# Optimization experiments

Hardware: AMD Instinct MI355X
Metric: run time of the kernel (lower is better)

The kernel has to match this reference:

```python
import jax, jax.numpy as jnp
import numpy as np

D_EMB = 1024
N_HEADS = 16
HEAD_DIM = D_EMB // N_HEADS


def _xavier(key, out_f, in_f):
    limit = jnp.sqrt(6.0 / (in_f + out_f))
    return jax.random.uniform(key, (out_f, in_f), jnp.float32, -limit, limit)


def setup_inputs() -> dict:
    key = jax.random.key(0)
    k_x, k_qkv, k_out = jax.random.split(key, 3)
    x = jax.random.normal(k_x, (4, 2048, D_EMB), jnp.float32)
    # torch nn.Linear weights: [out_features, in_features], xavier_uniform; biases zero
    w_qkv = _xavier(k_qkv, 3 * D_EMB, D_EMB)
    b_qkv = jnp.zeros((3 * D_EMB,), jnp.float32)
    w_out = _xavier(k_out, D_EMB, D_EMB)
    b_out = jnp.zeros((D_EMB,), jnp.float32)
    return {"x": x, "w_qkv": w_qkv, "b_qkv": b_qkv, "w_out": w_out, "b_out": b_out}


def reference(x, w_qkv, b_qkv, w_out, b_out):
    B, S, D = x.shape
    # QKV projection: y = x @ W^T + b -> [B, S, 3D]
    qkv = jnp.einsum('bsd,ed->bse', x, w_qkv) + b_qkv
    # view(B, S, H, 3*head_dim) then split into q, k, v (matches torch chunk on last dim)
    qkv = qkv.reshape(B, S, N_HEADS, 3 * HEAD_DIM)
    q, k, v = jnp.split(qkv, 3, axis=-1)  # each [B, S, H, head_dim]
    scale = 1.0 / jnp.sqrt(jnp.float32(HEAD_DIM))
    scores = jnp.einsum('bshd,bthd->bhst', q, k) * scale  # [B, H, S, S]
    probs = jax.nn.softmax(scores, axis=-1)
    out = jnp.einsum('bhst,bthd->bshd', probs, v).reshape(B, S, D)
    return jnp.einsum('bsd,ed->bse', out, w_out) + b_out
```

## Files before the change

### kernel.cpp

```cpp
#include <hip/hip_runtime.h>

typedef __bf16 bf16_t;
typedef __bf16 bf16x8 __attribute__((ext_vector_type(8)));
typedef __bf16 bf16x4 __attribute__((ext_vector_type(4)));
typedef float f32x4 __attribute__((ext_vector_type(4)));

#define S_LEN 2048
#define D_EMB 1024
#define NH 16

#define MFMA16(a, b, c) __builtin_amdgcn_mfma_f32_16x16x32_bf16((a), (b), (c), 0, 0, 0)

__device__ __forceinline__ void gld16(void* lds, const void* g) {
  __builtin_amdgcn_global_load_lds(
      (__attribute__((address_space(1))) void*)(void*)(g),
      (__attribute__((address_space(3))) void*)(lds), 16, 0, 0);
}

__device__ __forceinline__ float exp2_hw(float x) {
  float r;
  asm("v_exp_f32 %0, %1" : "=v"(r) : "v"(x));
  return r;
}

__global__ __launch_bounds__(256) void cvt_bf16(const float* __restrict__ in,
                                                bf16_t* __restrict__ out, int n4) {
  int i = blockIdx.x * 256 + threadIdx.x;
  if (i >= n4) return;
  float4 v = ((const float4*)in)[i];
  bf16x4 o;
  o[0] = (bf16_t)v.x; o[1] = (bf16_t)v.y; o[2] = (bf16_t)v.z; o[3] = (bf16_t)v.w;
  ((bf16x4*)out)[i] = o;
}

template <int EPI>
__global__ __launch_bounds__(256) void gemm_bt(
    const bf16_t* __restrict__ A, const bf16_t* __restrict__ W,
    const float* __restrict__ bias, float* __restrict__ outF,
    bf16_t* __restrict__ outQ, int M, int N, int K) {
  __shared__ __attribute__((aligned(16))) bf16_t As[128 * 64];
  __shared__ __attribute__((aligned(16))) bf16_t Ws[128 * 64];
  const int tid = threadIdx.x;
  const int lane = tid & 63;
  const int wid = tid >> 6;
  const int l15 = lane & 15, lg = lane >> 4;
  int lin = blockIdx.x + gridDim.x * blockIdx.y;
  const int nwg = gridDim.x * gridDim.y;
  lin = (lin & 7) * (nwg >> 3) + (lin >> 3);
  const int tm = (lin / gridDim.x) * 128, tn = (lin % gridDim.x) * 128;
  const int wm = (wid >> 1) * 64, wn = (wid & 1) * 64;
  f32x4 acc[4][4] = {};
  const int q0 = tid * 16;

  for (int k0 = 0; k0 < K; k0 += 64) {
#pragma unroll
    for (int i = 0; i < 4; ++i) {
      int q = q0 + i * 4096;
      int row = q >> 7;
      int scb = (q & 127) ^ ((row & 7) << 4);
      gld16((char*)As + (q & ~1023),
            (const char*)A + ((size_t)(tm + row) * K + k0) * 2 + scb);
      gld16((char*)Ws + (q & ~1023),
            (const char*)W + ((size_t)(tn + row) * K + k0) * 2 + scb);
    }
    __syncthreads();
#pragma unroll
    for (int kk = 0; kk < 2; ++kk) {
      const int cb = kk * 64 + lg * 16;
      bf16x8 af[4], bfr[4];
#pragma unroll
      for (int mi = 0; mi < 4; ++mi) {
        int row = wm + mi * 16 + l15;
        af[mi] = *(const bf16x8*)((const char*)As + row * 128 + (cb ^ ((row & 7) << 4)));
      }
#pragma unroll
      for (int ni = 0; ni < 4; ++ni) {
        int row = wn + ni * 16 + l15;
        bfr[ni] = *(const bf16x8*)((const char*)Ws + row * 128 + (cb ^ ((row & 7) << 4)));
      }
#pragma unroll
      for (int mi = 0; mi < 4; ++mi)
#pragma unroll
        for (int ni = 0; ni < 4; ++ni)
          acc[mi][ni] = MFMA16(af[mi], bfr[ni], acc[mi][ni]);
    }
    __syncthreads();
  }

  if (EPI == 0) {
#pragma unroll
    for (int mi = 0; mi < 4; ++mi)
#pragma unroll
      for (int ni = 0; ni < 4; ++ni) {
        int colg = tn + wn + ni * 16 + l15;
        float bv = bias[colg];
#pragma unroll
        for (int j = 0; j < 4; ++j) {
          int rowg = tm + wm + mi * 16 + lg * 4 + j;
          outF[(size_t)rowg * N + colg] = acc[mi][ni][j] + bv;
        }
      }
  } else {
#pragma unroll
    for (int mi = 0; mi < 4; ++mi)
#pragma unroll
      for (int ni = 0; ni < 4; ++ni) {
        int e = tn + wn + ni * 16 + l15;
        float bv = bias[e];
        int h = e / 192;
        int r = e - h * 192;
        int t = r >> 6, c = r & 63;
#pragma unroll
        for (int j = 0; j < 4; ++j) {
          int m = tm + wm + mi * 16 + lg * 4 + j;
          int b = m >> 11, s = m & 2047;
          float v = acc[mi][ni][j] + bv;
          if (t == 0) v *= 0.18033688011112042f;
          size_t base = ((size_t)(b * NH + h) * 3 + t) * (size_t)(S_LEN * 64);
          size_t idx;
          if (t == 2) {
            int rs = s & 31;
            int rp = (((rs >> 2) & 3) << 3) | ((rs >> 4) << 2) | (rs & 3);
            idx = base + (size_t)c * S_LEN + (size_t)((s & ~31) | rp);
          } else {
            idx = base + (size_t)s * 64 + c;
          }
          outQ[idx] = (bf16_t)v;
        }
      }
  }
}

__global__ __launch_bounds__(256) void attn_fwd(const bf16_t* __restrict__ qkvb,
                                                bf16_t* __restrict__ attnb) {
  __shared__ __attribute__((aligned(16))) bf16_t Ks[4][64 * 64];
  __shared__ __attribute__((aligned(16))) bf16_t Vs[4][64 * 64];
  const int tid = threadIdx.x, lane = tid & 63, wid = tid >> 6;
  const int l15 = lane & 15, lg = lane >> 4;
  int lin = blockIdx.x + (blockIdx.y << 4);
  lin = (lin & 7) * 128 + (lin >> 3);
  const int qt = lin & 15;
  const int bh = lin >> 4;
  const int b = bh >> 4, h = bh & 15;
  const char* Qg = (const char*)qkvb + (size_t)bh * 3 * (S_LEN * 64) * 2;
  const char* Kg = Qg + (size_t)S_LEN * 64 * 2;
  const char* Vtg = Kg + (size_t)S_LEN * 64 * 2;
  const int q0 = tid * 16;

  bf16x8 qf[2][2];
#pragma unroll
  for (int mi = 0; mi < 2; ++mi) {
    const char* qr = Qg + (size_t)(qt * 128 + wid * 32 + mi * 16 + l15) * 128;
#pragma unroll
    for (int kb = 0; kb < 2; ++kb)
      qf[mi][kb] = *(const bf16x8*)(qr + kb * 64 + lg * 16);
  }

  auto stage = [&](int t) {
#pragma unroll
    for (int i = 0; i < 2; ++i) {
      int q = q0 + i * 4096;
      int row = q >> 7;
      int scb = (q & 127) ^ ((row & 7) << 4);
      gld16((char*)Ks[t & 3] + (q & ~1023),
            Kg + (size_t)(t * 64 + row) * 128 + scb);
      gld16((char*)Vs[t & 3] + (q & ~1023),
            Vtg + (size_t)row * (S_LEN * 2) + t * 128 + scb);
    }
  };

  float lsum[2] = {0.f, 0.f};
  f32x4 o[2][4] = {};
  bf16x8 pf[2][2];
  const int swk = (l15 & 7) << 4;

  auto QK = [&](const bf16_t* Kc, f32x4(&stv)[2][4]) {
#pragma unroll
    for (int nk = 0; nk < 4; ++nk) {
      const char* kr = (const char*)Kc + (nk * 16 + l15) * 128;
      bf16x8 kf0 = *(const bf16x8*)(kr + ((lg * 16) ^ swk));
      bf16x8 kf1 = *(const bf16x8*)(kr + ((64 + lg * 16) ^ swk));
#pragma unroll
      for (int mi = 0; mi < 2; ++mi) {
        f32x4 z = {};
        z = MFMA16(kf0, qf[mi][0], z);
        stv[mi][nk] = MFMA16(kf1, qf[mi][1], z);
      }
    }
  };
  auto SM = [&](f32x4(&stv)[2][4]) {
#pragma unroll
    for (int mi = 0; mi < 2; ++mi)
#pragma unroll
      for (int nk = 0; nk < 4; ++nk)
#pragma unroll
        for (int j = 0; j < 4; ++j) {
          float p = exp2_hw(stv[mi][nk][j]);
          stv[mi][nk][j] = p;
          lsum[mi] += p;
        }
#pragma unroll
    for (int kp = 0; kp < 2; ++kp)
#pragma unroll
      for (int mi = 0; mi < 2; ++mi)
#pragma unroll
        for (int j = 0; j < 4; ++j) {
          pf[kp][mi][j] = (bf16_t)stv[mi][2 * kp][j];
          pf[kp][mi][4 + j] = (bf16_t)stv[mi][2 * kp + 1][j];
        }
  };
  auto PV = [&](const bf16_t* Vc) {
#pragma unroll
    for (int kp = 0; kp < 2; ++kp)
#pragma unroll
      for (int ndv = 0; ndv < 4; ++ndv) {
        const char* vr = (const char*)Vc + (ndv * 16 + l15) * 128;
        bf16x8 vf = *(const bf16x8*)(vr + ((kp * 64 + 16 * lg) ^ swk));
        o[0][ndv] = MFMA16(pf[kp][0], vf, o[0][ndv]);
        o[1][ndv] = MFMA16(pf[kp][1], vf, o[1][ndv]);
      }
  };

  stage(0); stage(1); stage(2);
  asm volatile("s_waitcnt vmcnt(8)" ::: "memory");
  __builtin_amdgcn_s_barrier();
  asm volatile("" ::: "memory");
  {
    f32x4 stv[2][4];
    __builtin_amdgcn_s_setprio(1);
    QK(Ks[0], stv);
    __builtin_amdgcn_s_setprio(0);
    SM(stv);
  }

  for (int kt = 0; kt < 30; ++kt) {
    asm volatile("s_waitcnt vmcnt(4)" ::: "memory");
    __builtin_amdgcn_s_barrier();
    asm volatile("" ::: "memory");
    if (kt + 3 < 32) stage(kt + 3);
    f32x4 stv[2][4];
    __builtin_amdgcn_s_setprio(1);
    QK(Ks[(kt + 1) & 3], stv);
    PV(Vs[kt & 3]);
    __builtin_amdgcn_s_setprio(0);
    SM(stv);
  }
  asm volatile("s_waitcnt vmcnt(0)" ::: "memory");
  __builtin_amdgcn_s_barrier();
  asm volatile("" ::: "memory");
  {
    f32x4 stv[2][4];
    __builtin_amdgcn_s_setprio(1);
    QK(Ks[31 & 3], stv);
    PV(Vs[30 & 3]);
    __builtin_amdgcn_s_setprio(0);
    SM(stv);
  }
  PV(Vs[31 & 3]);

#pragma unroll
  for (int mi = 0; mi < 2; ++mi) {
    lsum[mi] += __shfl_xor(lsum[mi], 16);
    lsum[mi] += __shfl_xor(lsum[mi], 32);
  }
  float inv[2][4];
#pragma unroll
  for (int mi = 0; mi < 2; ++mi)
#pragma unroll
    for (int j = 0; j < 4; ++j)
      inv[mi][j] = 1.0f / __shfl(lsum[mi], (lane & 48) | (lg * 4 + j));

#pragma unroll
  for (int mi = 0; mi < 2; ++mi)
#pragma unroll
    for (int j = 0; j < 4; ++j) {
      int srow = qt * 128 + wid * 32 + mi * 16 + lg * 4 + j;
      bf16_t* dst = attnb + ((size_t)b * S_LEN + srow) * D_EMB + h * 64;
#pragma unroll
      for (int ndv = 0; ndv < 4; ++ndv)
        dst[ndv * 16 + l15] = (bf16_t)(o[mi][ndv][j] * inv[mi][j]);
    }
}

extern "C" void kernel_launch(void* const* d_in, const int* in_sizes, int n_in,
                              void* d_out, int out_size, void* d_ws, size_t ws_size,
                              hipStream_t stream) {
  const float* x = (const float*)d_in[0];
  const float* w_qkv = (const float*)d_in[1];
  const float* b_qkv = (const float*)d_in[2];
  const float* w_out = (const float*)d_in[3];
  const float* b_out = (const float*)d_in[4];
  float* out = (float*)d_out;

  bf16_t* xb = (bf16_t*)d_ws;
  bf16_t* wqkvb = xb + 8388608;
  bf16_t* woutb = wqkvb + 3145728;
  bf16_t* qkvb = woutb + 1048576;
  bf16_t* attnb = qkvb + 25165824;

  cvt_bf16<<<8192, 256, 0, stream>>>(x, xb, 2097152);
  cvt_bf16<<<3072, 256, 0, stream>>>(w_qkv, wqkvb, 786432);
  cvt_bf16<<<1024, 256, 0, stream>>>(w_out, woutb, 262144);

  gemm_bt<1><<<dim3(24, 64), 256, 0, stream>>>(xb, wqkvb, b_qkv, nullptr, qkvb,
                                               8192, 3072, 1024);
  attn_fwd<<<dim3(16, 64), 256, 0, stream>>>(qkvb, attnb);
  gemm_bt<0><<<dim3(8, 64), 256, 0, stream>>>(attnb, woutb, b_out, out, nullptr,
                                              8192, 1024, 1024);
}
```

Baseline: 205.2 us.

## Compute softmax denominator via MFMA with ones and shrink K/V LDS ring to three stages

The attention kernel drops the per-element scalar sum of exp values and instead gets the row denominators from extra MFMA instructions that multiply the bf16 probabilities by a ones vector. This removes the VALU adds and the final cross-lane shuffles. It also splits K and V staging so V is loaded one tile later, and cuts the LDS ring from four to three buffers to lower shared-memory use and possibly raise occupancy. The trade-off is extra MFMA work, and the denominator now sums bf16-rounded probabilities, which matches the numerator.

```diff
diff --git a/kernel.cpp b/kernel.cpp
--- a/kernel.cpp
+++ b/kernel.cpp
@@ -133,8 +133,8 @@
 
 __global__ __launch_bounds__(256) void attn_fwd(const bf16_t* __restrict__ qkvb,
                                                 bf16_t* __restrict__ attnb) {
-  __shared__ __attribute__((aligned(16))) bf16_t Ks[4][64 * 64];
-  __shared__ __attribute__((aligned(16))) bf16_t Vs[4][64 * 64];
+  __shared__ __attribute__((aligned(16))) bf16_t Ks[3][64 * 64];
+  __shared__ __attribute__((aligned(16))) bf16_t Vs[3][64 * 64];
   const int tid = threadIdx.x, lane = tid & 63, wid = tid >> 6;
   const int l15 = lane & 15, lg = lane >> 4;
   int lin = blockIdx.x + (blockIdx.y << 4);
@@ -156,22 +156,32 @@
       qf[mi][kb] = *(const bf16x8*)(qr + kb * 64 + lg * 16);
   }
 
-  auto stage = [&](int t) {
+  auto stageK = [&](int t) {
 #pragma unroll
     for (int i = 0; i < 2; ++i) {
       int q = q0 + i * 4096;
       int row = q >> 7;
       int scb = (q & 127) ^ ((row & 7) << 4);
-      gld16((char*)Ks[t & 3] + (q & ~1023),
-            Kg + (size_t)(t * 64 + row) * 128 + scb);
-      gld16((char*)Vs[t & 3] + (q & ~1023),
+      gld16((char*)Ks[t % 3] + (q & ~1023), Kg + (size_t)(t * 64 + row) * 128 + scb);
+    }
+  };
+  auto stageV = [&](int t) {
+#pragma unroll
+    for (int i = 0; i < 2; ++i) {
+      int q = q0 + i * 4096;
+      int row = q >> 7;
+      int scb = (q & 127) ^ ((row & 7) << 4);
+      gld16((char*)Vs[t % 3] + (q & ~1023),
             Vtg + (size_t)row * (S_LEN * 2) + t * 128 + scb);
     }
   };
 
-  float lsum[2] = {0.f, 0.f};
   f32x4 o[2][4] = {};
+  f32x4 den[2] = {};
   bf16x8 pf[2][2];
+  bf16x8 onesf;
+#pragma unroll
+  for (int j = 0; j < 8; ++j) onesf[j] = (bf16_t)1.0f;
   const int swk = (l15 & 7) << 4;
 
   auto QK = [&](const bf16_t* Kc, f32x4(&stv)[2][4]) {
@@ -194,11 +204,8 @@
 #pragma unroll
       for (int nk = 0; nk < 4; ++nk)
 #pragma unroll
-        for (int j = 0; j < 4; ++j) {
-          float p = exp2_hw(stv[mi][nk][j]);
-          stv[mi][nk][j] = p;
-          lsum[mi] += p;
-        }
+        for (int j = 0; j < 4; ++j)
+          stv[mi][nk][j] = exp2_hw(stv[mi][nk][j]);
 #pragma unroll
     for (int kp = 0; kp < 2; ++kp)
 #pragma unroll
@@ -211,7 +218,7 @@
   };
   auto PV = [&](const bf16_t* Vc) {
 #pragma unroll
-    for (int kp = 0; kp < 2; ++kp)
+    for (int kp = 0; kp < 2; ++kp) {
 #pragma unroll
       for (int ndv = 0; ndv < 4; ++ndv) {
         const char* vr = (const char*)Vc + (ndv * 16 + l15) * 128;
@@ -219,10 +226,13 @@
         o[0][ndv] = MFMA16(pf[kp][0], vf, o[0][ndv]);
         o[1][ndv] = MFMA16(pf[kp][1], vf, o[1][ndv]);
       }
-  };
-
-  stage(0); stage(1); stage(2);
-  asm volatile("s_waitcnt vmcnt(8)" ::: "memory");
+      den[0] = MFMA16(pf[kp][0], onesf, den[0]);
+      den[1] = MFMA16(pf[kp][1], onesf, den[1]);
+    }
+  };
+
+  stageV(0); stageK(0); stageV(1); stageK(1); stageK(2);
+  asm volatile("s_waitcnt vmcnt(6)" ::: "memory");
   __builtin_amdgcn_s_barrier();
   asm volatile("" ::: "memory");
   {
@@ -234,14 +244,15 @@
   }
 
   for (int kt = 0; kt < 30; ++kt) {
-    asm volatile("s_waitcnt vmcnt(4)" ::: "memory");
+    asm volatile("s_waitcnt vmcnt(2)" ::: "memory");
     __builtin_amdgcn_s_barrier();
     asm volatile("" ::: "memory");
-    if (kt + 3 < 32) stage(kt + 3);
+    stageV(kt + 2);
+    if (kt + 3 < 32) stageK(kt + 3);
     f32x4 stv[2][4];
     __builtin_amdgcn_s_setprio(1);
-    QK(Ks[(kt + 1) & 3], stv);
-    PV(Vs[kt & 3]);
+    QK(Ks[(kt + 1) % 3], stv);
+    PV(Vs[kt % 3]);
     __builtin_amdgcn_s_setprio(0);
     SM(stv);
   }
@@ -251,24 +262,19 @@
   {
     f32x4 stv[2][4];
     __builtin_amdgcn_s_setprio(1);
-    QK(Ks[31 & 3], stv);
-    PV(Vs[30 & 3]);
+    QK(Ks[31 % 3], stv);
+    PV(Vs[30 % 3]);
     __builtin_amdgcn_s_setprio(0);
     SM(stv);
   }
-  PV(Vs[31 & 3]);
-
-#pragma unroll
-  for (int mi = 0; mi < 2; ++mi) {
-    lsum[mi] += __shfl_xor(lsum[mi], 16);
-    lsum[mi] += __shfl_xor(lsum[mi], 32);
-  }
+  PV(Vs[31 % 3]);
+
   float inv[2][4];
 #pragma unroll
   for (int mi = 0; mi < 2; ++mi)
 #pragma unroll
     for (int j = 0; j < 4; ++j)
-      inv[mi][j] = 1.0f / __shfl(lsum[mi], (lane & 48) | (lg * 4 + j));
+      inv[mi][j] = 1.0f / den[mi][j];
 
 #pragma unroll
   for (int mi = 0; mi < 2; ++mi)
```

After: 200.4 us. 1.02x faster.
